# Kernel optimization log

Measured on AMD Instinct MI355X. Metric: run time of the kernel, lower is better.

## Reference

```python
import jax, jax.numpy as jnp
import numpy as np

CO, NO, ITERATIONS, STRIDE = 32, 8, 3, 2


def _squash(x, axis):
    norm = jnp.linalg.norm(x, axis=axis, keepdims=True)
    return x * norm / (1.0 + norm ** 2)


def _quantize(x, bits):
    # Faithful instantiation: identity quantization (full-precision pass-through),
    # matching running the original module with quantization_function = lambda t, b: t.
    return x


def setup_inputs() -> dict:
    key = jax.random.key(0)
    k1, k2, k3 = jax.random.split(key, 3)
    x = jax.random.normal(k1, (16, 256, 1, 20, 20), dtype=jnp.float32)
    W = jax.random.normal(k2, (CO * NO, 1, 9, 9), dtype=jnp.float32) * 0.05  # Conv2d weight [co*no, ni, k, k]
    bias = jax.random.normal(k3, (CO, NO, 1, 1), dtype=jnp.float32) * 0.01
    return {"x": x, "W": W, "bias": bias,
            "quantization_bits": 8, "quantization_bits_routing": 8}


def reference(x, W, bias, quantization_bits, quantization_bits_routing):
    bs, ci, ni, hi, wi = x.shape
    # vote generation: conv over each input capsule channel independently
    lhs = x.reshape(bs * ci, ni, hi, wi)
    votes = jax.lax.conv_general_dilated(
        lhs, W, window_strides=(STRIDE, STRIDE), padding='VALID',
        dimension_numbers=('NCHW', 'OIHW', 'NCHW'))
    votes = _quantize(votes, quantization_bits)
    ho, wo = votes.shape[-2:]
    votes = votes.reshape(bs, ci, CO, NO, ho, wo)  # [bs, ci, co, no, ho, wo]

    logits = jnp.zeros((bs, ci, CO, ho, wo), dtype=votes.dtype)
    activation = None
    for _ in range(ITERATIONS):
        route = jax.nn.softmax(logits, axis=2)                      # c_ij over co
        route = _quantize(route, quantization_bits)
        # s_j = sum_i c_ij * u_hat_{j|i} + bias  -> [bs, co, no, ho, wo]
        preactivate = jnp.einsum('bichw,bicnhw->bcnhw', route, votes) + bias
        preactivate = _quantize(preactivate, quantization_bits_routing)
        activation = _squash(preactivate, axis=2)                   # squash over no
        activation = _quantize(activation, quantization_bits)
        # agreement: <u_hat_{j|i}, v_j> summed over no -> [bs, ci, co, ho, wo]
        distances = jnp.einsum('bicnhw,bcnhw->bichw', votes, activation)
        logits = _quantize(logits + distances, quantization_bits_routing)
    return activation
```

## Files before the change

kernel.cpp:

```cpp
#include <hip/hip_runtime.h>


#define BS 16
#define CI 256
#define CO 32
#define NO 8
#define HI 20
#define WI 20
#define HO 6
#define WO 6
#define NPIX 36
#define NTAP 81
#define XP 104
#define NBLK 256

typedef __attribute__((ext_vector_type(8))) short bf16x8;
typedef __attribute__((ext_vector_type(4))) float f32x4;

__device__ __forceinline__ ushort f2bf(float x) {
    union { float f; unsigned u; } v; v.f = x;
    unsigned r = v.u + 0x7FFFu + ((v.u >> 16) & 1u);
    return (ushort)(r >> 16);
}

template<int CTRL>
__device__ __forceinline__ float dpp_radd(float v) {
    int s = __builtin_amdgcn_update_dpp(0, __float_as_int(v), CTRL, 0xF, 0xF, true);
    return v + __int_as_float(s);
}
__device__ __forceinline__ float row16_sum_tail(float v) {
    v = dpp_radd<0x111>(v);
    v = dpp_radd<0x112>(v);
    v = dpp_radd<0x114>(v);
    v = dpp_radd<0x118>(v);
    return v;
}
__device__ __forceinline__ float grp8_sum_all(float v) {
    v = dpp_radd<0xB1>(v);
    v = dpp_radd<0x4E>(v);
    v = dpp_radd<0x141>(v);
    return v;
}
#if __has_builtin(__builtin_amdgcn_permlane16_swap)
typedef unsigned u32x2 __attribute__((ext_vector_type(2)));
__device__ __forceinline__ float xor16_sum(float v) {
    u32x2 r = __builtin_amdgcn_permlane16_swap(__float_as_uint(v), __float_as_uint(v), false, false);
    return __uint_as_float(r.x) + __uint_as_float(r.y);
}
#else
__device__ __forceinline__ float xor16_sum(float v) { return v + __shfl_xor(v, 16, 64); }
#endif
#if __has_builtin(__builtin_amdgcn_permlane32_swap)
typedef unsigned u32x2b __attribute__((ext_vector_type(2)));
__device__ __forceinline__ float xor32_sum(float v) {
    u32x2b r = __builtin_amdgcn_permlane32_swap(__float_as_uint(v), __float_as_uint(v), false, false);
    return __uint_as_float(r.x) + __uint_as_float(r.y);
}
#else
__device__ __forceinline__ float xor32_sum(float v) { return v + __shfl_xor(v, 32, 64); }
#endif

__device__ __forceinline__ void stage_x(const float* __restrict__ xb,
                                        ushort* __restrict__ xw,
                                        int t, int h, int w) {
    const int w2 = 2 * w;
    #pragma unroll
    for (int pass = 0; pass < 9; ++pass) {
        int idx = pass * 1024 + t;
        int q4 = idx & 3, r = idx >> 2;
        int kh = r % 9, i = r / 9;
        float4 v = *(const float4*)(xb + (i * HI + 2 * h + kh) * WI + 4 * q4);
        const float* ve = &v.x;
        #pragma unroll
        for (int e = 0; e < 4; ++e) {
            int kw = 4 * q4 + e - w2;
            if ((unsigned)kw < 9u) xw[i * XP + kh * 9 + kw] = f2bf(ve[e]);
        }
    }
    if (w >= 4) {
        for (int r = t; r < CI * 9; r += 1024) {
            int kh = r % 9, i = r / 9;
            float4 v = *(const float4*)(xb + (i * HI + 2 * h + kh) * WI + 16);
            const float* ve = &v.x;
            #pragma unroll
            for (int e = 0; e < 4; ++e) {
                int kw = 16 + e - w2;
                if ((unsigned)kw < 9u) xw[i * XP + kh * 9 + kw] = f2bf(ve[e]);
            }
        }
    }
}

__global__ __launch_bounds__(1024) void caps_kernel(
    const float* __restrict__ x,
    const float* __restrict__ Wt,
    const float* __restrict__ bias,
    float* __restrict__ out)
{
    __shared__ __align__(16) ushort xw[CI * XP];
    __shared__ __align__(16) ushort wl[CO * NO * XP];
    __shared__ __align__(16) float  smx[4 * 256];
    __shared__ __align__(16) float  pre[4 * 256];
    __shared__ __align__(16) float  act[256];

    const int t   = threadIdx.x, blk = blockIdx.x;
    const int b   = blk & 15;
    const int npix = (blk < 64) ? 3 : 2;
    const float* xb = x + b * CI * HI * WI;

    const int wid = t >> 6, l = t & 63;
    const int q = l >> 4, il = l & 15;
    const int wf = wid >> 2, wi = wid & 3;

    for (int p = t; p < CO * NO * NTAP; p += 1024) {
        int f = p / NTAP, k = p - f * NTAP;
        wl[f * XP + k] = f2bf(Wt[p]);
    }
    {
        int i = t >> 2, s4 = t & 3;
        #pragma unroll
        for (int j = 0; j < 6; ++j) {
            int k = NTAP + s4 * 6 + j;
            if (k < XP) { xw[i * XP + k] = 0; wl[i * XP + k] = 0; }
        }
    }
    stage_x(xb, xw, t, (blk >> 4) / WO, (blk >> 4) % WO);

    const float bias_r = (t < 256) ? bias[t] : 0.f;

    for (int p = 0; p < npix; ++p) {
        const int hw = (blk + 256 * p) >> 4;
        const int h  = hw / WO, w = hw % WO;

        __syncthreads();

        f32x4 acc[4][4];
        #pragma unroll
        for (int tf = 0; tf < 4; ++tf)
            #pragma unroll
            for (int ti = 0; ti < 4; ++ti)
                acc[tf][ti] = (f32x4){0.f, 0.f, 0.f, 0.f};

        #pragma unroll
        for (int ks = 0; ks < 3; ++ks) {
            const int ko = ks * 32 + q * 8;
            bf16x8 af[4], bv[4];
            #pragma unroll
            for (int tf = 0; tf < 4; ++tf)
                af[tf] = *(const bf16x8*)&wl[(wf * 64 + tf * 16 + il) * XP + ko];
            #pragma unroll
            for (int ti = 0; ti < 4; ++ti)
                bv[ti] = *(const bf16x8*)&xw[(wi * 64 + ti * 16 + il) * XP + ko];
            #pragma unroll
            for (int tf = 0; tf < 4; ++tf)
                #pragma unroll
                for (int ti = 0; ti < 4; ++ti)
                    acc[tf][ti] = __builtin_amdgcn_mfma_f32_16x16x32_bf16(
                        af[tf], bv[ti], acc[tf][ti], 0, 0, 0);
        }

        __syncthreads();

        if (p + 1 < npix) {
            const int hwn = (blk + 256 * (p + 1)) >> 4;
            stage_x(xb, xw, t, hwn / WO, hwn % WO);
        }

        float lg[4][4];
        #pragma unroll
        for (int tf = 0; tf < 4; ++tf)
            #pragma unroll
            for (int ti = 0; ti < 4; ++ti) lg[tf][ti] = 0.f;

        #pragma unroll
        for (int it = 0; it < 3; ++it) {
            float pp[4][4];
            if (it == 0) {
                #pragma unroll
                for (int tf = 0; tf < 4; ++tf)
                    #pragma unroll
                    for (int r = 0; r < 4; ++r)
                        pp[tf][r] = (acc[tf][0][r] + acc[tf][1][r]
                                   + acc[tf][2][r] + acc[tf][3][r]) * 0.03125f;
            } else {
                float e[4][4], srow[4] = {0.f, 0.f, 0.f, 0.f};
                #pragma unroll
                for (int tf = 0; tf < 4; ++tf)
                    #pragma unroll
                    for (int ti = 0; ti < 4; ++ti) {
                        e[tf][ti] = __expf(lg[tf][ti]);
                        srow[ti] += e[tf][ti];
                    }
                #pragma unroll
                for (int ti = 0; ti < 4; ++ti)
                    srow[ti] = xor32_sum(srow[ti]);
                if (q == 0) {
                    #pragma unroll
                    for (int ti = 0; ti < 4; ++ti)
                        smx[wf * 256 + wi * 64 + ti * 16 + il] = srow[ti];
                }
                __syncthreads();
                float rtot[4];
                #pragma unroll
                for (int ti = 0; ti < 4; ++ti) {
                    int i = wi * 64 + ti * 16 + il;
                    rtot[ti] = __builtin_amdgcn_rcpf(
                        smx[i] + smx[256 + i] + smx[512 + i] + smx[768 + i]);
                }
                float route[4][4];
                #pragma unroll
                for (int tf = 0; tf < 4; ++tf)
                    #pragma unroll
                    for (int ti = 0; ti < 4; ++ti) route[tf][ti] = e[tf][ti] * rtot[ti];
                #pragma unroll
                for (int tf = 0; tf < 4; ++tf)
                    #pragma unroll
                    for (int r = 0; r < 4; ++r)
                        pp[tf][r] = route[tf][0] * acc[tf][0][r] + route[tf][1] * acc[tf][1][r]
                                  + route[tf][2] * acc[tf][2][r] + route[tf][3] * acc[tf][3][r];
            }

            #pragma unroll
            for (int tf = 0; tf < 4; ++tf)
                #pragma unroll
                for (int r = 0; r < 4; ++r)
                    pp[tf][r] = row16_sum_tail(pp[tf][r]);
            if (il == 15) {
                #pragma unroll
                for (int tf = 0; tf < 4; ++tf) {
                    int c = wf * 8 + tf * 2 + (q >> 1);
                    f32x4 vv = {pp[tf][0], pp[tf][1], pp[tf][2], pp[tf][3]};
                    *(f32x4*)&pre[wi * 256 + c * 8 + (q & 1) * 4] = vv;
                }
            }
            __syncthreads();

            if (t < 256) {
                float s = bias_r + pre[t] + pre[256 + t] + pre[512 + t] + pre[768 + t];
                float sq = grp8_sum_all(s * s);
                float a = s * __builtin_amdgcn_sqrtf(sq) * __builtin_amdgcn_rcpf(1.f + sq);
                if (it == 2) {
                    int c = t >> 3, n = t & 7;
                    out[(((b * CO + c) * NO + n) * HO + h) * WO + w] = a;
                } else {
                    act[t] = a;
                }
            }

            if (it < 2) {
                __syncthreads();
                #pragma unroll
                for (int tf = 0; tf < 4; ++tf) {
                    int c = wf * 8 + tf * 2 + (q >> 1);
                    f32x4 av = *(const f32x4*)&act[c * 8 + (q & 1) * 4];
                    #pragma unroll
                    for (int ti = 0; ti < 4; ++ti) {
                        float d = acc[tf][ti][0] * av[0] + acc[tf][ti][1] * av[1]
                                + acc[tf][ti][2] * av[2] + acc[tf][ti][3] * av[3];
                        lg[tf][ti] += xor16_sum(d);
                    }
                }
            }
        }
    }
}

extern "C" void kernel_launch(void* const* d_in, const int* in_sizes, int n_in,
                              void* d_out, int out_size, void* d_ws, size_t ws_size,
                              hipStream_t stream) {
    const float* x    = (const float*)d_in[0];
    const float* Wt   = (const float*)d_in[1];
    const float* bias = (const float*)d_in[2];
    float* out = (float*)d_out;
    caps_kernel<<<NBLK, 1024, 0, stream>>>(x, Wt, bias, out);
}
```

Measured before the change: 57.20 us.

## Split capsule routing into one-pixel blocks with global bf16 weights

Adds a small pre-kernel that converts the conv weights to padded bf16 in the workspace. The main kernel now launches one 512-thread block per (batch, pixel), 576 blocks in all, and reads weight fragments straight from global memory instead of staging them in LDS. Votes are kept in registers packed as bf16 pairs. Removing the weight tile from LDS cuts shared-memory use, which allows several blocks per CU and removes the per-pixel restaging loop. The cost is an extra launch, global/L2 traffic for weight loads, and lower precision for the routing votes. A fallback one-pixel 1024-thread kernel runs when the workspace is too small.

```diff
diff --git a/kernel.cpp b/kernel.cpp
--- a/kernel.cpp
+++ b/kernel.cpp
@@ -12,7 +12,8 @@
 #define NPIX 36
 #define NTAP 81
 #define XP 104
-#define NBLK 256
+#define KW 96
+#define NBLK 576
 
 typedef __attribute__((ext_vector_type(8))) short bf16x8;
 typedef __attribute__((ext_vector_type(4))) float f32x4;
@@ -22,6 +23,11 @@
     unsigned r = v.u + 0x7FFFu + ((v.u >> 16) & 1u);
     return (ushort)(r >> 16);
 }
+__device__ __forceinline__ unsigned packbf(float a, float b) {
+    return (unsigned)f2bf(a) | ((unsigned)f2bf(b) << 16);
+}
+__device__ __forceinline__ float bflo(unsigned u) { return __uint_as_float(u << 16); }
+__device__ __forceinline__ float bfhi(unsigned u) { return __uint_as_float(u & 0xFFFF0000u); }
 
 template<int CTRL>
 __device__ __forceinline__ float dpp_radd(float v) {
@@ -60,13 +66,38 @@
 __device__ __forceinline__ float xor32_sum(float v) { return v + __shfl_xor(v, 32, 64); }
 #endif
 
-__device__ __forceinline__ void stage_x(const float* __restrict__ xb,
-                                        ushort* __restrict__ xw,
-                                        int t, int h, int w) {
-    const int w2 = 2 * w;
-    #pragma unroll
-    for (int pass = 0; pass < 9; ++pass) {
-        int idx = pass * 1024 + t;
+__global__ __launch_bounds__(256) void prep_w(const float* __restrict__ Wt,
+                                              ushort* __restrict__ wb) {
+    int idx = blockIdx.x * 256 + threadIdx.x;
+    int f = idx / KW, k = idx - f * KW;
+    wb[idx] = (k < NTAP) ? f2bf(Wt[f * NTAP + k]) : (ushort)0;
+}
+
+__global__ __launch_bounds__(512, 4) void caps512_kernel(
+    const ushort* __restrict__ wb,
+    const float* __restrict__ x,
+    const float* __restrict__ bias,
+    float* __restrict__ out)
+{
+    __shared__ __align__(16) ushort xw[CI * XP];
+    __shared__ __align__(16) float  smx[4 * 256];
+    __shared__ __align__(16) float  pre[2 * 256];
+    __shared__ __align__(16) float  act[256];
+
+    const int t   = threadIdx.x, blk = blockIdx.x;
+    const int b   = blk & 15;
+    const int hw  = blk >> 4;
+    const int h   = hw / WO, w = hw % WO;
+    const int w2  = 2 * w;
+    const float* xb = x + b * CI * HI * WI;
+
+    const int wid = t >> 6, l = t & 63;
+    const int q = l >> 4, il = l & 15;
+    const int wf = wid >> 1, wi = wid & 1;
+
+    #pragma unroll
+    for (int pass = 0; pass < 18; ++pass) {
+        int idx = pass * 512 + t;
         int q4 = idx & 3, r = idx >> 2;
         int kh = r % 9, i = r / 9;
         float4 v = *(const float4*)(xb + (i * HI + 2 * h + kh) * WI + 4 * q4);
@@ -78,7 +109,7 @@
         }
     }
     if (w >= 4) {
-        for (int r = t; r < CI * 9; r += 1024) {
+        for (int r = t; r < CI * 9; r += 512) {
             int kh = r % 9, i = r / 9;
             float4 v = *(const float4*)(xb + (i * HI + 2 * h + kh) * WI + 16);
             const float* ve = &v.x;
@@ -89,13 +120,170 @@
             }
         }
     }
-}
-
-__global__ __launch_bounds__(1024) void caps_kernel(
-    const float* __restrict__ x,
-    const float* __restrict__ Wt,
-    const float* __restrict__ bias,
-    float* __restrict__ out)
+    {
+        int i = t >> 1, s = t & 1;
+        #pragma unroll
+        for (int j = 0; j < 12; ++j) {
+            int k = NTAP + s * 12 + j;
+            if (k < XP) { xw[i * XP + k] = 0; xw[(i + 128) * XP + k] = 0; }
+        }
+    }
+
+    const float bias_r = (t < 256) ? bias[t] : 0.f;
+    __syncthreads();
+
+    unsigned pv[4][4][2][2];
+    #pragma unroll
+    for (int p = 0; p < 4; ++p) {
+        f32x4 acc[4][2];
+        #pragma unroll
+        for (int tf = 0; tf < 4; ++tf)
+            #pragma unroll
+            for (int ti2 = 0; ti2 < 2; ++ti2)
+                acc[tf][ti2] = (f32x4){0.f, 0.f, 0.f, 0.f};
+        #pragma unroll
+        for (int ks = 0; ks < 3; ++ks) {
+            const int ko = ks * 32 + q * 8;
+            bf16x8 af[4], bv[2];
+            #pragma unroll
+            for (int tf = 0; tf < 4; ++tf)
+                af[tf] = *(const bf16x8*)&wb[(wf * 64 + tf * 16 + il) * KW + ko];
+            #pragma unroll
+            for (int ti2 = 0; ti2 < 2; ++ti2)
+                bv[ti2] = *(const bf16x8*)&xw[(wi * 128 + p * 32 + ti2 * 16 + il) * XP + ko];
+            #pragma unroll
+            for (int tf = 0; tf < 4; ++tf)
+                #pragma unroll
+                for (int ti2 = 0; ti2 < 2; ++ti2)
+                    acc[tf][ti2] = __builtin_amdgcn_mfma_f32_16x16x32_bf16(
+                        af[tf], bv[ti2], acc[tf][ti2], 0, 0, 0);
+        }
+        #pragma unroll
+        for (int tf = 0; tf < 4; ++tf)
+            #pragma unroll
+            for (int ti2 = 0; ti2 < 2; ++ti2) {
+                pv[p][tf][ti2][0] = packbf(acc[tf][ti2][0], acc[tf][ti2][1]);
+                pv[p][tf][ti2][1] = packbf(acc[tf][ti2][2], acc[tf][ti2][3]);
+            }
+    }
+
+    float lg[4][4][2];
+    #pragma unroll
+    for (int tf = 0; tf < 4; ++tf)
+        #pragma unroll
+        for (int p = 0; p < 4; ++p)
+            #pragma unroll
+            for (int ti2 = 0; ti2 < 2; ++ti2) lg[tf][p][ti2] = 0.f;
+
+    #pragma unroll
+    for (int it = 0; it < 3; ++it) {
+        float pp[4][4];
+        #pragma unroll
+        for (int tf = 0; tf < 4; ++tf)
+            #pragma unroll
+            for (int r = 0; r < 4; ++r) pp[tf][r] = 0.f;
+
+        if (it == 0) {
+            #pragma unroll
+            for (int p = 0; p < 4; ++p)
+                #pragma unroll
+                for (int ti2 = 0; ti2 < 2; ++ti2)
+                    #pragma unroll
+                    for (int tf = 0; tf < 4; ++tf) {
+                        unsigned u0 = pv[p][tf][ti2][0], u1 = pv[p][tf][ti2][1];
+                        pp[tf][0] += bflo(u0); pp[tf][1] += bfhi(u0);
+                        pp[tf][2] += bflo(u1); pp[tf][3] += bfhi(u1);
+                    }
+            #pragma unroll
+            for (int tf = 0; tf < 4; ++tf)
+                #pragma unroll
+                for (int r = 0; r < 4; ++r) pp[tf][r] *= 0.03125f;
+        } else {
+            float srow[4][2];
+            #pragma unroll
+            for (int p = 0; p < 4; ++p)
+                #pragma unroll
+                for (int ti2 = 0; ti2 < 2; ++ti2) {
+                    float s = 0.f;
+                    #pragma unroll
+                    for (int tf = 0; tf < 4; ++tf) s += __expf(lg[tf][p][ti2]);
+                    srow[p][ti2] = xor32_sum(s);
+                }
+            if (q == 0) {
+                #pragma unroll
+                for (int p = 0; p < 4; ++p)
+                    #pragma unroll
+                    for (int ti2 = 0; ti2 < 2; ++ti2)
+                        smx[wf * 256 + wi * 128 + p * 32 + ti2 * 16 + il] = srow[p][ti2];
+            }
+            __syncthreads();
+            #pragma unroll
+            for (int p = 0; p < 4; ++p)
+                #pragma unroll
+                for (int ti2 = 0; ti2 < 2; ++ti2) {
+                    const int i = wi * 128 + p * 32 + ti2 * 16 + il;
+                    const float rt = __builtin_amdgcn_rcpf(
+                        smx[i] + smx[256 + i] + smx[512 + i] + smx[768 + i]);
+                    #pragma unroll
+                    for (int tf = 0; tf < 4; ++tf) {
+                        const float route = __expf(lg[tf][p][ti2]) * rt;
+                        unsigned u0 = pv[p][tf][ti2][0], u1 = pv[p][tf][ti2][1];
+                        pp[tf][0] += route * bflo(u0); pp[tf][1] += route * bfhi(u0);
+                        pp[tf][2] += route * bflo(u1); pp[tf][3] += route * bfhi(u1);
+                    }
+                }
+        }
+
+        #pragma unroll
+        for (int tf = 0; tf < 4; ++tf)
+            #pragma unroll
+            for (int r = 0; r < 4; ++r)
+                pp[tf][r] = row16_sum_tail(pp[tf][r]);
+        if (il == 15) {
+            #pragma unroll
+            for (int tf = 0; tf < 4; ++tf) {
+                int c = wf * 8 + tf * 2 + (q >> 1);
+                f32x4 vv = {pp[tf][0], pp[tf][1], pp[tf][2], pp[tf][3]};
+                *(f32x4*)&pre[wi * 256 + c * 8 + (q & 1) * 4] = vv;
+            }
+        }
+        __syncthreads();
+
+        if (t < 256) {
+            float s = bias_r + pre[t] + pre[256 + t];
+            float sq = grp8_sum_all(s * s);
+            float a = s * __builtin_amdgcn_sqrtf(sq) * __builtin_amdgcn_rcpf(1.f + sq);
+            if (it == 2) {
+                int c = t >> 3, n = t & 7;
+                out[((b * CO + c) * NO + n) * NPIX + hw] = a;
+            } else {
+                act[t] = a;
+            }
+        }
+
+        if (it < 2) {
+            __syncthreads();
+            #pragma unroll
+            for (int tf = 0; tf < 4; ++tf) {
+                const int c = wf * 8 + tf * 2 + (q >> 1);
+                f32x4 av = *(const f32x4*)&act[c * 8 + (q & 1) * 4];
+                #pragma unroll
+                for (int p = 0; p < 4; ++p)
+                    #pragma unroll
+                    for (int ti2 = 0; ti2 < 2; ++ti2) {
+                        unsigned u0 = pv[p][tf][ti2][0], u1 = pv[p][tf][ti2][1];
+                        float d = bflo(u0) * av[0] + bfhi(u0) * av[1]
+                                + bflo(u1) * av[2] + bfhi(u1) * av[3];
+                        lg[tf][p][ti2] += xor16_sum(d);
+                    }
+            }
+        }
+    }
+}
+
+__global__ __launch_bounds__(1024) void caps_kernel_r7(
+    const float* __restrict__ x, const float* __restrict__ Wt,
+    const float* __restrict__ bias, float* __restrict__ out)
 {
     __shared__ __align__(16) ushort xw[CI * XP];
     __shared__ __align__(16) ushort wl[CO * NO * XP];
@@ -103,13 +291,10 @@
     __shared__ __align__(16) float  pre[4 * 256];
     __shared__ __align__(16) float  act[256];
 
-    const int t   = threadIdx.x, blk = blockIdx.x;
-    const int b   = blk & 15;
-    const int npix = (blk < 64) ? 3 : 2;
-    const float* xb = x + b * CI * HI * WI;
-
-    const int wid = t >> 6, l = t & 63;
-    const int q = l >> 4, il = l & 15;
+    const int t = threadIdx.x, blk = blockIdx.x;
+    const int b = blk & 15, hw = blk >> 4;
+    const int h = hw / WO, w = hw % WO, w2 = 2 * w;
+    const int wid = t >> 6, l = t & 63, q = l >> 4, il = l & 15;
     const int wf = wid >> 2, wi = wid & 3;
 
     for (int p = t; p < CO * NO * NTAP; p += 1024) {
@@ -124,141 +309,143 @@
             if (k < XP) { xw[i * XP + k] = 0; wl[i * XP + k] = 0; }
         }
     }
-    stage_x(xb, xw, t, (blk >> 4) / WO, (blk >> 4) % WO);
-
+    #pragma unroll
+    for (int pass = 0; pass < 9; ++pass) {
+        int idx = pass * 1024 + t;
+        int q4 = idx & 3, r = idx >> 2;
+        int kh = r % 9, i = r / 9;
+        float4 v = *(const float4*)(x + ((b * CI + i) * HI + (2 * h + kh)) * WI + 4 * q4);
+        const float* ve = &v.x;
+        #pragma unroll
+        for (int e = 0; e < 4; ++e) {
+            int kw = 4 * q4 + e - w2;
+            if ((unsigned)kw < 9u) xw[i * XP + kh * 9 + kw] = f2bf(ve[e]);
+        }
+    }
+    if (w >= 4) {
+        for (int r = t; r < CI * 9; r += 1024) {
+            int kh = r % 9, i = r / 9;
+            float4 v = *(const float4*)(x + ((b * CI + i) * HI + (2 * h + kh)) * WI + 16);
+            const float* ve = &v.x;
+            #pragma unroll
+            for (int e = 0; e < 4; ++e) {
+                int kw = 16 + e - w2;
+                if ((unsigned)kw < 9u) xw[i * XP + kh * 9 + kw] = f2bf(ve[e]);
+            }
+        }
+    }
     const float bias_r = (t < 256) ? bias[t] : 0.f;
-
-    for (int p = 0; p < npix; ++p) {
-        const int hw = (blk + 256 * p) >> 4;
-        const int h  = hw / WO, w = hw % WO;
-
+    __syncthreads();
+
+    f32x4 acc[4][4];
+    #pragma unroll
+    for (int tf = 0; tf < 4; ++tf)
+        #pragma unroll
+        for (int ti = 0; ti < 4; ++ti) acc[tf][ti] = (f32x4){0.f, 0.f, 0.f, 0.f};
+    #pragma unroll
+    for (int ks = 0; ks < 3; ++ks) {
+        const int ko = ks * 32 + q * 8;
+        bf16x8 af[4], bv[4];
+        #pragma unroll
+        for (int tf = 0; tf < 4; ++tf)
+            af[tf] = *(const bf16x8*)&wl[(wf * 64 + tf * 16 + il) * XP + ko];
+        #pragma unroll
+        for (int ti = 0; ti < 4; ++ti)
+            bv[ti] = *(const bf16x8*)&xw[(wi * 64 + ti * 16 + il) * XP + ko];
+        #pragma unroll
+        for (int tf = 0; tf < 4; ++tf)
+            #pragma unroll
+            for (int ti = 0; ti < 4; ++ti)
+                acc[tf][ti] = __builtin_amdgcn_mfma_f32_16x16x32_bf16(
+                    af[tf], bv[ti], acc[tf][ti], 0, 0, 0);
+    }
+
+    float lg[4][4];
+    #pragma unroll
+    for (int tf = 0; tf < 4; ++tf)
+        #pragma unroll
+        for (int ti = 0; ti < 4; ++ti) lg[tf][ti] = 0.f;
+
+    #pragma unroll
+    for (int it = 0; it < 3; ++it) {
+        float pp[4][4];
+        if (it == 0) {
+            #pragma unroll
+            for (int tf = 0; tf < 4; ++tf)
+                #pragma unroll
+                for (int r = 0; r < 4; ++r)
+                    pp[tf][r] = (acc[tf][0][r] + acc[tf][1][r]
+                               + acc[tf][2][r] + acc[tf][3][r]) * 0.03125f;
+        } else {
+            float e[4][4], srow[4] = {0.f, 0.f, 0.f, 0.f};
+            #pragma unroll
+            for (int tf = 0; tf < 4; ++tf)
+                #pragma unroll
+                for (int ti = 0; ti < 4; ++ti) {
+                    e[tf][ti] = __expf(lg[tf][ti]);
+                    srow[ti] += e[tf][ti];
+                }
+            #pragma unroll
+            for (int ti = 0; ti < 4; ++ti) srow[ti] = xor32_sum(srow[ti]);
+            if (q == 0) {
+                #pragma unroll
+                for (int ti = 0; ti < 4; ++ti)
+                    smx[wf * 256 + wi * 64 + ti * 16 + il] = srow[ti];
+            }
+            __syncthreads();
+            float rtot[4];
+            #pragma unroll
+            for (int ti = 0; ti < 4; ++ti) {
+                int i = wi * 64 + ti * 16 + il;
+                rtot[ti] = __builtin_amdgcn_rcpf(
+                    smx[i] + smx[256 + i] + smx[512 + i] + smx[768 + i]);
+            }
+            float route[4][4];
+            #pragma unroll
+            for (int tf = 0; tf < 4; ++tf)
+                #pragma unroll
+                for (int ti = 0; ti < 4; ++ti) route[tf][ti] = e[tf][ti] * rtot[ti];
+            #pragma unroll
+            for (int tf = 0; tf < 4; ++tf)
+                #pragma unroll
+                for (int r = 0; r < 4; ++r)
+                    pp[tf][r] = route[tf][0] * acc[tf][0][r] + route[tf][1] * acc[tf][1][r]
+                              + route[tf][2] * acc[tf][2][r] + route[tf][3] * acc[tf][3][r];
+        }
+        #pragma unroll
+        for (int tf = 0; tf < 4; ++tf)
+            #pragma unroll
+            for (int r = 0; r < 4; ++r)
+                pp[tf][r] = row16_sum_tail(pp[tf][r]);
+        if (il == 15) {
+            #pragma unroll
+            for (int tf = 0; tf < 4; ++tf) {
+                int c = wf * 8 + tf * 2 + (q >> 1);
+                f32x4 vv = {pp[tf][0], pp[tf][1], pp[tf][2], pp[tf][3]};
+                *(f32x4*)&pre[wi * 256 + c * 8 + (q & 1) * 4] = vv;
+            }
+        }
         __syncthreads();
-
-        f32x4 acc[4][4];
-        #pragma unroll
-        for (int tf = 0; tf < 4; ++tf)
-            #pragma unroll
-            for (int ti = 0; ti < 4; ++ti)
-                acc[tf][ti] = (f32x4){0.f, 0.f, 0.f, 0.f};
-
-        #pragma unroll
-        for (int ks = 0; ks < 3; ++ks) {
-            const int ko = ks * 32 + q * 8;
-            bf16x8 af[4], bv[4];
-            #pragma unroll
-            for (int tf = 0; tf < 4; ++tf)
-                af[tf] = *(const bf16x8*)&wl[(wf * 64 + tf * 16 + il) * XP + ko];
-            #pragma unroll
-            for (int ti = 0; ti < 4; ++ti)
-                bv[ti] = *(const bf16x8*)&xw[(wi * 64 + ti * 16 + il) * XP + ko];
-            #pragma unroll
-            for (int tf = 0; tf < 4; ++tf)
-                #pragma unroll
-                for (int ti = 0; ti < 4; ++ti)
-                    acc[tf][ti] = __builtin_amdgcn_mfma_f32_16x16x32_bf16(
-                        af[tf], bv[ti], acc[tf][ti], 0, 0, 0);
-        }
-
-        __syncthreads();
-
-        if (p + 1 < npix) {
-            const int hwn = (blk + 256 * (p + 1)) >> 4;
-            stage_x(xb, xw, t, hwn / WO, hwn % WO);
-        }
-
-        float lg[4][4];
-        #pragma unroll
-        for (int tf = 0; tf < 4; ++tf)
-            #pragma unroll
-            for (int ti = 0; ti < 4; ++ti) lg[tf][ti] = 0.f;
-
-        #pragma unroll
-        for (int it = 0; it < 3; ++it) {
-            float pp[4][4];
-            if (it == 0) {
-                #pragma unroll
-                for (int tf = 0; tf < 4; ++tf)
-                    #pragma unroll
-                    for (int r = 0; r < 4; ++r)
-                        pp[tf][r] = (acc[tf][0][r] + acc[tf][1][r]
-                                   + acc[tf][2][r] + acc[tf][3][r]) * 0.03125f;
-            } else {
-                float e[4][4], srow[4] = {0.f, 0.f, 0.f, 0.f};
-                #pragma unroll
-                for (int tf = 0; tf < 4; ++tf)
-                    #pragma unroll
-                    for (int ti = 0; ti < 4; ++ti) {
-                        e[tf][ti] = __expf(lg[tf][ti]);
-                        srow[ti] += e[tf][ti];
-                    }
-                #pragma unroll
-                for (int ti = 0; ti < 4; ++ti)
-                    srow[ti] = xor32_sum(srow[ti]);
-                if (q == 0) {
-                    #pragma unroll
-                    for (int ti = 0; ti < 4; ++ti)
-                        smx[wf * 256 + wi * 64 + ti * 16 + il] = srow[ti];
-                }
-                __syncthreads();
-                float rtot[4];
+        if (t < 256) {
+            float s = bias_r + pre[t] + pre[256 + t] + pre[512 + t] + pre[768 + t];
+            float sq = grp8_sum_all(s * s);
+            float a = s * __builtin_amdgcn_sqrtf(sq) * __builtin_amdgcn_rcpf(1.f + sq);
+            if (it == 2) {
+                int c = t >> 3, n = t & 7;
+                out[(((b * CO + c) * NO + n) * HO + h) * WO + w] = a;
+            } else act[t] = a;
+        }
+        if (it < 2) {
+            __syncthreads();
+            #pragma unroll
+            for (int tf = 0; tf < 4; ++tf) {
+                int c = wf * 8 + tf * 2 + (q >> 1);
+                f32x4 av = *(const f32x4*)&act[c * 8 + (q & 1) * 4];
                 #pragma unroll
                 for (int ti = 0; ti < 4; ++ti) {
-                    int i = wi * 64 + ti * 16 + il;
-                    rtot[ti] = __builtin_amdgcn_rcpf(
-                        smx[i] + smx[256 + i] + smx[512 + i] + smx[768 + i]);
-                }
-                float route[4][4];
-                #pragma unroll
-                for (int tf = 0; tf < 4; ++tf)
-                    #pragma unroll
-                    for (int ti = 0; ti < 4; ++ti) route[tf][ti] = e[tf][ti] * rtot[ti];
-                #pragma unroll
-                for (int tf = 0; tf < 4; ++tf)
-                    #pragma unroll
-                    for (int r = 0; r < 4; ++r)
-                        pp[tf][r] = route[tf][0] * acc[tf][0][r] + route[tf][1] * acc[tf][1][r]
-                                  + route[tf][2] * acc[tf][2][r] + route[tf][3] * acc[tf][3][r];
-            }
-
-            #pragma unroll
-            for (int tf = 0; tf < 4; ++tf)
-                #pragma unroll
-                for (int r = 0; r < 4; ++r)
-                    pp[tf][r] = row16_sum_tail(pp[tf][r]);
-            if (il == 15) {
-                #pragma unroll
-                for (int tf = 0; tf < 4; ++tf) {
-                    int c = wf * 8 + tf * 2 + (q >> 1);
-                    f32x4 vv = {pp[tf][0], pp[tf][1], pp[tf][2], pp[tf][3]};
-                    *(f32x4*)&pre[wi * 256 + c * 8 + (q & 1) * 4] = vv;
-                }
-            }
-            __syncthreads();
-
-            if (t < 256) {
-                float s = bias_r + pre[t] + pre[256 + t] + pre[512 + t] + pre[768 + t];
-                float sq = grp8_sum_all(s * s);
-                float a = s * __builtin_amdgcn_sqrtf(sq) * __builtin_amdgcn_rcpf(1.f + sq);
-                if (it == 2) {
-                    int c = t >> 3, n = t & 7;
-                    out[(((b * CO + c) * NO + n) * HO + h) * WO + w] = a;
-                } else {
-                    act[t] = a;
-                }
-            }
-
-            if (it < 2) {
-                __syncthreads();
-                #pragma unroll
-                for (int tf = 0; tf < 4; ++tf) {
-                    int c = wf * 8 + tf * 2 + (q >> 1);
-                    f32x4 av = *(const f32x4*)&act[c * 8 + (q & 1) * 4];
-                    #pragma unroll
-                    for (int ti = 0; ti < 4; ++ti) {
-                        float d = acc[tf][ti][0] * av[0] + acc[tf][ti][1] * av[1]
-                                + acc[tf][ti][2] * av[2] + acc[tf][ti][3] * av[3];
-                        lg[tf][ti] += xor16_sum(d);
-                    }
+                    float d = acc[tf][ti][0] * av[0] + acc[tf][ti][1] * av[1]
+                            + acc[tf][ti][2] * av[2] + acc[tf][ti][3] * av[3];
+                    lg[tf][ti] += xor16_sum(d);
                 }
             }
         }
@@ -272,5 +459,12 @@
     const float* Wt   = (const float*)d_in[1];
     const float* bias = (const float*)d_in[2];
     float* out = (float*)d_out;
-    caps_kernel<<<NBLK, 1024, 0, stream>>>(x, Wt, bias, out);
-}
+
+    if (ws_size >= (size_t)256 * KW * sizeof(ushort)) {
+        ushort* wb = (ushort*)d_ws;
+        prep_w<<<96, 256, 0, stream>>>(Wt, wb);
+        caps512_kernel<<<NBLK, 512, 0, stream>>>(wb, x, bias, out);
+    } else {
+        caps_kernel_r7<<<NBLK, 1024, 0, stream>>>(x, Wt, bias, out);
+    }
+}
```

Result: slower. 206.4 us (+260.8%).
